# Performance work log

Measured on AMD Instinct MI355X. Metric: run time of the kernel, lower is better.

## Reference

```python
import jax, jax.numpy as jnp
import numpy as np

WH, WW = 8, 8           # window size
NUM_HEADS = 6
DIM = 192
BW = 4096               # num_windows * batch
NW = 64                 # windows per image (mask leading dim)
N = WH * WW             # tokens per window = 64


def _make_rel_coords_table():
    h = np.arange(-(WH - 1), WH, dtype=np.float32)
    w = np.arange(-(WW - 1), WW, dtype=np.float32)
    gh, gw = np.meshgrid(h, w, indexing='ij')
    tbl = np.stack([gh, gw], axis=-1)[None]            # (1, 2Wh-1, 2Ww-1, 2)
    tbl[..., 0] /= (WH - 1)
    tbl[..., 1] /= (WW - 1)
    tbl *= 8.0
    tbl = np.sign(tbl) * np.log2(np.abs(tbl) + 1.0) / np.log2(8.0)
    return jnp.asarray(tbl, dtype=jnp.float32)


def _make_rel_pos_index():
    ch, cw = np.meshgrid(np.arange(WH), np.arange(WW), indexing='ij')
    coords = np.stack([ch, cw]).reshape(2, -1)          # (2, N)
    rel = coords[:, :, None] - coords[:, None, :]       # (2, N, N)
    rel = rel.transpose(1, 2, 0)
    rel[..., 0] += WH - 1
    rel[..., 1] += WW - 1
    rel[..., 0] *= 2 * WW - 1
    return jnp.asarray(rel.sum(-1), dtype=jnp.int64)    # (N, N)


def setup_inputs() -> dict:
    key = jax.random.key(0)
    ks = jax.random.split(key, 8)
    s = 0.02
    return {
        'x': jax.random.normal(ks[0], (BW, N, DIM), dtype=jnp.float32),
        'mask': jnp.zeros((NW, N, N), dtype=jnp.float32),
        'qkv_w': jax.random.normal(ks[1], (3 * DIM, DIM), dtype=jnp.float32) * s,
        'q_bias': jnp.zeros((DIM,), dtype=jnp.float32),
        'v_bias': jnp.zeros((DIM,), dtype=jnp.float32),
        'logit_scale': jnp.log(10.0 * jnp.ones((NUM_HEADS, 1, 1), dtype=jnp.float32)),
        'cpb_w1': jax.random.normal(ks[2], (512, 2), dtype=jnp.float32) * s,
        'cpb_b1': jnp.zeros((512,), dtype=jnp.float32),
        'cpb_w2': jax.random.normal(ks[3], (NUM_HEADS, 512), dtype=jnp.float32) * s,
        'proj_w': jax.random.normal(ks[4], (DIM, DIM), dtype=jnp.float32) * s,
        'proj_b': jnp.zeros((DIM,), dtype=jnp.float32),
        'rel_coords_table': _make_rel_coords_table(),
        'rel_pos_index': _make_rel_pos_index(),
    }


def reference(x, mask, qkv_w, q_bias, v_bias, logit_scale, cpb_w1, cpb_b1,
              cpb_w2, proj_w, proj_b, rel_coords_table, rel_pos_index):
    B_, n, C = x.shape
    H = logit_scale.shape[0]
    d = C // H
    # qkv projection; k has no bias (zeros), matching the torch concat
    qkv_bias = jnp.concatenate([q_bias, jnp.zeros_like(v_bias), v_bias])
    qkv = x @ qkv_w.T + qkv_bias                              # (B_, n, 3C)
    qkv = qkv.reshape(B_, n, 3, H, d).transpose(2, 0, 3, 1, 4)  # (3, B_, H, n, d)
    q, k, v = qkv[0], qkv[1], qkv[2]
    # cosine attention: L2-normalize q, k (eps like F.normalize)
    qn = q / jnp.clip(jnp.linalg.norm(q, axis=-1, keepdims=True), 1e-12)
    kn = k / jnp.clip(jnp.linalg.norm(k, axis=-1, keepdims=True), 1e-12)
    attn = jnp.einsum('bhnd,bhmd->bhnm', qn, kn)              # (B_, H, n, n)
    max_log = jnp.log(jnp.asarray(100.0, dtype=logit_scale.dtype))
    scale = jnp.exp(jnp.minimum(logit_scale, max_log))        # (H,1,1)
    attn = attn * scale
    # continuous position bias via small MLP, gathered by relative index
    hidden = jax.nn.relu(rel_coords_table @ cpb_w1.T + cpb_b1)
    tbl = (hidden @ cpb_w2.T).reshape(-1, H)                  # ((2Wh-1)(2Ww-1), H)
    rpb = tbl[rel_pos_index.reshape(-1)].reshape(n, n, H).transpose(2, 0, 1)
    rpb = 16.0 * jax.nn.sigmoid(rpb)                          # (H, n, n)
    attn = attn + rpb[None]
    nW = mask.shape[0]
    attn = attn.reshape(B_ // nW, nW, H, n, n) + mask[None, :, None]
    attn = jax.nn.softmax(attn.reshape(B_, H, n, n), axis=-1)
    out = jnp.einsum('bhnm,bhmd->bhnd', attn, v)
    out = out.transpose(0, 2, 1, 3).reshape(B_, n, C)
    return out @ proj_w.T + proj_b
```

## Files before the change

### kernel.cpp

```cpp
#include <hip/hip_runtime.h>


#define LDA 200
#define LDV 72
#define LDP 72

typedef __attribute__((ext_vector_type(4))) float floatx4;
typedef __attribute__((ext_vector_type(8))) short shortx8;
typedef __attribute__((ext_vector_type(4))) unsigned short ushortx4;

__device__ __forceinline__ unsigned short f2bf(float f) {
    union { float f; unsigned u; } v; v.f = f;
    return (unsigned short)((v.u + 0x7fffu + ((v.u >> 16) & 1u)) >> 16);
}
__device__ __forceinline__ float bf2f(unsigned short s) {
    union { unsigned u; float f; } v; v.u = ((unsigned)s) << 16;
    return v.f;
}

__global__ void prep_weights(const float* __restrict__ qkv_w,
                             const float* __restrict__ proj_w,
                             const float* __restrict__ q_bias,
                             const float* __restrict__ v_bias,
                             unsigned short* __restrict__ qkvw_bf,
                             unsigned short* __restrict__ projw_bf,
                             float* __restrict__ qkvb) {
    int stride = gridDim.x * blockDim.x;
    for (int i = blockIdx.x * blockDim.x + threadIdx.x; i < 110592 + 36864 + 576; i += stride) {
        if (i < 110592) {
            qkvw_bf[i] = f2bf(qkv_w[i]);
        } else if (i < 110592 + 36864) {
            projw_bf[i - 110592] = f2bf(proj_w[i - 110592]);
        } else {
            int j = i - 110592 - 36864;
            qkvb[j] = (j < 192) ? q_bias[j] : (j < 384 ? 0.f : v_bias[j - 384]);
        }
    }
}

__global__ void prep_cpb_tbl(const float* __restrict__ w1, const float* __restrict__ b1,
                             const float* __restrict__ w2, const float* __restrict__ rct,
                             float* __restrict__ tbls) {
    int wave = threadIdx.x >> 6, lane = threadIdx.x & 63;
    int pr = blockIdx.x * 4 + wave;
    if (pr >= 1350) return;
    int p = pr / 6, h = pr - p * 6;
    float c0 = rct[p * 2], c1 = rct[p * 2 + 1];
    float s = 0.f;
    #pragma unroll
    for (int it = 0; it < 8; ++it) {
        int j = lane + it * 64;
        float hv = fmaxf(0.f, c0 * w1[j * 2] + c1 * w1[j * 2 + 1] + b1[j]);
        s += hv * w2[h * 512 + j];
    }
    #pragma unroll
    for (int off = 32; off >= 1; off >>= 1) s += __shfl_xor(s, off);
    if (lane == 0) tbls[pr] = s;
}

__global__ void prep_cpb_gather(const float* __restrict__ tbls, const int* __restrict__ rpi,
                                float* __restrict__ rpb) {
    int e = blockIdx.x * 256 + threadIdx.x;
    if (e >= 24576) return;
    int stride64 = (rpi[1] == 0) ? 2 : 1;
    int h = e >> 12, rc = e & 4095;
    int idx = rpi[rc * stride64];
    float t = tbls[idx * 6 + h];
    rpb[e] = 16.f / (1.f + __expf(-t));
}

__global__ __launch_bounds__(768, 3) void win_attn(
    const float* __restrict__ x, const float* __restrict__ mask,
    const float* __restrict__ logit_scale,
    const unsigned short* __restrict__ qkvw, const unsigned short* __restrict__ projw,
    const float* __restrict__ qkvb, const float* __restrict__ projb,
    const float* __restrict__ rpb, float* __restrict__ out)
{
    __shared__ unsigned short Xs[64 * LDA];
    __shared__ unsigned short Qs[64 * LDA];
    __shared__ unsigned short Ks[64 * LDA];
    __shared__ unsigned short Vt[192 * LDV];
    __shared__ unsigned short Ps[12][16 * LDP];

    const int tid  = threadIdx.x;
    const int b    = blockIdx.x;
    const int wave = tid >> 6, lane = tid & 63;
    const int c = lane & 15, qd = lane >> 4;

    {
        const float4* xw = (const float4*)(x + (size_t)b * 12288);
        for (int i = tid; i < 3072; i += 768) {
            float4 v = xw[i];
            int token = i / 48, c4 = (i - token * 48) * 4;
            ushortx4 u = { f2bf(v.x), f2bf(v.y), f2bf(v.z), f2bf(v.w) };
            *(ushortx4*)&Xs[token * LDA + c4] = u;
        }
    }
    __syncthreads();

    {
        for (int nti = 0; nti < 3; ++nti) {
            int nt = wave * 3 + nti;
            const unsigned short* bp = qkvw + (nt * 16 + c) * 192 + qd * 8;
            shortx8 bf[6];
            #pragma unroll
            for (int ks = 0; ks < 6; ++ks) bf[ks] = *(const shortx8*)(bp + ks * 32);
            int gcol = nt * 16 + c;
            int part = nt / 12;
            int inner = gcol - part * 192;
            float bias = qkvb[gcol];
            #pragma unroll
            for (int mh = 0; mh < 2; ++mh) {
                shortx8 af[2][6];
                #pragma unroll
                for (int mi = 0; mi < 2; ++mi)
                    #pragma unroll
                    for (int ks = 0; ks < 6; ++ks)
                        af[mi][ks] = *(const shortx8*)&Xs[((mh * 2 + mi) * 16 + c) * LDA + ks * 32 + qd * 8];
                floatx4 acc[2];
                acc[0] = (floatx4){0.f, 0.f, 0.f, 0.f};
                acc[1] = (floatx4){0.f, 0.f, 0.f, 0.f};
                #pragma unroll
                for (int ks = 0; ks < 6; ++ks)
                    #pragma unroll
                    for (int mi = 0; mi < 2; ++mi)
                        acc[mi] = __builtin_amdgcn_mfma_f32_16x16x32_bf16(af[mi][ks], bf[ks], acc[mi], 0, 0, 0);
                #pragma unroll
                for (int mi = 0; mi < 2; ++mi)
                    #pragma unroll
                    for (int r = 0; r < 4; ++r) {
                        int row = (mh * 2 + mi) * 16 + qd * 4 + r;
                        unsigned short bv = f2bf(acc[mi][r] + bias);
                        if (part == 2) Vt[inner * LDV + row] = bv;
                        else if (part == 1) Ks[row * LDA + inner] = bv;
                        else Qs[row * LDA + inner] = bv;
                    }
            }
        }
    }
    __syncthreads();

    {
        int idx = tid;
        int pqk = idx / 384, rem = idx - pqk * 384;
        int h = rem >> 6, token = rem & 63;
        unsigned short* p = (pqk == 0 ? Qs : Ks) + token * LDA + h * 32;
        shortx8 v0 = *(shortx8*)(p),      v1 = *(shortx8*)(p + 8),
                v2 = *(shortx8*)(p + 16), v3 = *(shortx8*)(p + 24);
        float s = 0.f;
        #pragma unroll
        for (int j = 0; j < 8; ++j) {
            float f0 = bf2f((unsigned short)v0[j]), f1 = bf2f((unsigned short)v1[j]);
            float f2 = bf2f((unsigned short)v2[j]), f3 = bf2f((unsigned short)v3[j]);
            s += f0 * f0 + f1 * f1 + f2 * f2 + f3 * f3;
        }
        float rn = 1.f / fmaxf(sqrtf(s), 1e-12f);
        if (pqk == 0) rn *= __expf(fminf(logit_scale[h], 4.605170185988091f));
        #pragma unroll
        for (int j = 0; j < 8; ++j) {
            v0[j] = (short)f2bf(bf2f((unsigned short)v0[j]) * rn);
            v1[j] = (short)f2bf(bf2f((unsigned short)v1[j]) * rn);
            v2[j] = (short)f2bf(bf2f((unsigned short)v2[j]) * rn);
            v3[j] = (short)f2bf(bf2f((unsigned short)v3[j]) * rn);
        }
        *(shortx8*)(p) = v0; *(shortx8*)(p + 8) = v1;
        *(shortx8*)(p + 16) = v2; *(shortx8*)(p + 24) = v3;
    }
    __syncthreads();

    {
        const float* maskw = mask + (size_t)(b & 63) * 4096;
        const int h = wave >> 1;
        const float* rpbh = rpb + h * 4096;
        shortx8 kf[4];
        #pragma unroll
        for (int nt = 0; nt < 4; ++nt)
            kf[nt] = *(const shortx8*)&Ks[(nt * 16 + c) * LDA + h * 32 + qd * 8];
        shortx8 vf[2][2];
        #pragma unroll
        for (int kn = 0; kn < 2; ++kn)
            #pragma unroll
            for (int nd = 0; nd < 2; ++nd)
                vf[kn][nd] = *(const shortx8*)&Vt[(h * 32 + nd * 16 + c) * LDV + kn * 32 + qd * 8];
        #pragma unroll
        for (int mti = 0; mti < 2; ++mti) {
            int mt = (wave & 1) * 2 + mti;
            float rm[4][4];
            #pragma unroll
            for (int r = 0; r < 4; ++r) {
                int row = mt * 16 + qd * 4 + r;
                #pragma unroll
                for (int nt = 0; nt < 4; ++nt) {
                    int col = nt * 16 + c;
                    rm[r][nt] = rpbh[row * 64 + col] + maskw[row * 64 + col];
                }
            }
            shortx8 qf = *(const shortx8*)&Qs[(mt * 16 + c) * LDA + h * 32 + qd * 8];
            floatx4 a[4];
            #pragma unroll
            for (int nt = 0; nt < 4; ++nt) {
                floatx4 z = (floatx4){0.f, 0.f, 0.f, 0.f};
                a[nt] = __builtin_amdgcn_mfma_f32_16x16x32_bf16(qf, kf[nt], z, 0, 0, 0);
            }
            #pragma unroll
            for (int r = 0; r < 4; ++r) {
                float vals[4], vmax = -1e30f;
                #pragma unroll
                for (int nt = 0; nt < 4; ++nt) {
                    float v = a[nt][r] + rm[r][nt];
                    vals[nt] = v; vmax = fmaxf(vmax, v);
                }
                #pragma unroll
                for (int off = 1; off < 16; off <<= 1)
                    vmax = fmaxf(vmax, __shfl_xor(vmax, off, 16));
                float ssum = 0.f;
                #pragma unroll
                for (int nt = 0; nt < 4; ++nt) {
                    float e = __expf(vals[nt] - vmax);
                    vals[nt] = e; ssum += e;
                }
                #pragma unroll
                for (int off = 1; off < 16; off <<= 1)
                    ssum += __shfl_xor(ssum, off, 16);
                float inv = 1.f / ssum;
                #pragma unroll
                for (int nt = 0; nt < 4; ++nt)
                    Ps[wave][(qd * 4 + r) * LDP + nt * 16 + c] = f2bf(vals[nt] * inv);
            }
            asm volatile("s_waitcnt lgkmcnt(0)" ::: "memory");
            shortx8 pf[2];
            #pragma unroll
            for (int kn = 0; kn < 2; ++kn)
                pf[kn] = *(const shortx8*)&Ps[wave][c * LDP + kn * 32 + qd * 8];
            #pragma unroll
            for (int nd = 0; nd < 2; ++nd) {
                floatx4 o = (floatx4){0.f, 0.f, 0.f, 0.f};
                o = __builtin_amdgcn_mfma_f32_16x16x32_bf16(pf[0], vf[0][nd], o, 0, 0, 0);
                o = __builtin_amdgcn_mfma_f32_16x16x32_bf16(pf[1], vf[1][nd], o, 0, 0, 0);
                #pragma unroll
                for (int r = 0; r < 4; ++r)
                    Xs[(mt * 16 + qd * 4 + r) * LDA + h * 32 + nd * 16 + c] = f2bf(o[r]);
            }
        }
    }
    __syncthreads();

    {
        const int nt = wave;
        const unsigned short* bp = projw + (nt * 16 + c) * 192 + qd * 8;
        shortx8 bf[6];
        #pragma unroll
        for (int ks = 0; ks < 6; ++ks) bf[ks] = *(const shortx8*)(bp + ks * 32);
        int gcol = nt * 16 + c;
        float bias = projb[gcol];
        float* outw = out + (size_t)b * 12288;
        #pragma unroll
        for (int mh = 0; mh < 2; ++mh) {
            shortx8 af[2][6];
            #pragma unroll
            for (int mi = 0; mi < 2; ++mi)
                #pragma unroll
                for (int ks = 0; ks < 6; ++ks)
                    af[mi][ks] = *(const shortx8*)&Xs[((mh * 2 + mi) * 16 + c) * LDA + ks * 32 + qd * 8];
            floatx4 acc[2];
            acc[0] = (floatx4){0.f, 0.f, 0.f, 0.f};
            acc[1] = (floatx4){0.f, 0.f, 0.f, 0.f};
            #pragma unroll
            for (int ks = 0; ks < 6; ++ks)
                #pragma unroll
                for (int mi = 0; mi < 2; ++mi)
                    acc[mi] = __builtin_amdgcn_mfma_f32_16x16x32_bf16(af[mi][ks], bf[ks], acc[mi], 0, 0, 0);
            #pragma unroll
            for (int mi = 0; mi < 2; ++mi)
                #pragma unroll
                for (int r = 0; r < 4; ++r)
                    outw[((mh * 2 + mi) * 16 + qd * 4 + r) * 192 + gcol] = acc[mi][r] + bias;
        }
    }
}

extern "C" void kernel_launch(void* const* d_in, const int* in_sizes, int n_in,
                              void* d_out, int out_size, void* d_ws, size_t ws_size,
                              hipStream_t stream) {
    const float* x           = (const float*)d_in[0];
    const float* mask        = (const float*)d_in[1];
    const float* qkv_w       = (const float*)d_in[2];
    const float* q_bias      = (const float*)d_in[3];
    const float* v_bias      = (const float*)d_in[4];
    const float* logit_scale = (const float*)d_in[5];
    const float* cpb_w1      = (const float*)d_in[6];
    const float* cpb_b1      = (const float*)d_in[7];
    const float* cpb_w2      = (const float*)d_in[8];
    const float* proj_w      = (const float*)d_in[9];
    const float* proj_b      = (const float*)d_in[10];
    const float* rct         = (const float*)d_in[11];
    const int*   rpi         = (const int*)d_in[12];

    char* ws = (char*)d_ws;
    unsigned short* qkvw_bf  = (unsigned short*)ws;
    unsigned short* projw_bf = (unsigned short*)(ws + 221184);
    float* qkvb = (float*)(ws + 294912);
    float* rpb  = (float*)(ws + 297216);
    float* tbls = (float*)(ws + 395520);

    prep_weights<<<64, 256, 0, stream>>>(qkv_w, proj_w, q_bias, v_bias, qkvw_bf, projw_bf, qkvb);
    prep_cpb_tbl<<<338, 256, 0, stream>>>(cpb_w1, cpb_b1, cpb_w2, rct, tbls);
    prep_cpb_gather<<<96, 256, 0, stream>>>(tbls, rpi, rpb);
    win_attn<<<4096, 768, 0, stream>>>(x, mask, logit_scale, qkvw_bf, projw_bf,
                                       qkvb, proj_b, rpb, (float*)d_out);
}
```

Before: 590.1 us.

## Spill K/V to global scratch, defer cosine normalization to scores, shrink LDS

K and V projections are no longer kept in LDS. They go to a per-window scratch area inside the output buffer, in MFMA-friendly layouts, and the Ks/Vt shared arrays are removed. Q/K normalization no longer rewrites the vectors. Per-token inverse norms go to LDS and are applied to the QK^T scores. Projection input now reuses Qs, and the launch-bounds occupancy hint is raised. The goal is to cut LDS per block so more blocks can share a CU, at the cost of an extra global/L2 round trip for K and V and possible register pressure from the tighter bound.

```diff
diff --git a/kernel.cpp b/kernel.cpp
--- a/kernel.cpp
+++ b/kernel.cpp
@@ -2,7 +2,6 @@
 
 
 #define LDA 200
-#define LDV 72
 #define LDP 72
 
 typedef __attribute__((ext_vector_type(4))) float floatx4;
@@ -69,7 +68,7 @@
     rpb[e] = 16.f / (1.f + __expf(-t));
 }
 
-__global__ __launch_bounds__(768, 3) void win_attn(
+__global__ __launch_bounds__(768, 6) void win_attn(
     const float* __restrict__ x, const float* __restrict__ mask,
     const float* __restrict__ logit_scale,
     const unsigned short* __restrict__ qkvw, const unsigned short* __restrict__ projw,
@@ -78,14 +77,15 @@
 {
     __shared__ unsigned short Xs[64 * LDA];
     __shared__ unsigned short Qs[64 * LDA];
-    __shared__ unsigned short Ks[64 * LDA];
-    __shared__ unsigned short Vt[192 * LDV];
     __shared__ unsigned short Ps[12][16 * LDP];
 
     const int tid  = threadIdx.x;
     const int b    = blockIdx.x;
     const int wave = tid >> 6, lane = tid & 63;
     const int c = lane & 15, qd = lane >> 4;
+
+    unsigned short* kv = (unsigned short*)(out + (size_t)b * 12288);
+    float* nrm = (float*)Xs;
 
     {
         const float4* xw = (const float4*)(x + (size_t)b * 12288);
@@ -126,28 +126,42 @@
                     for (int mi = 0; mi < 2; ++mi)
                         acc[mi] = __builtin_amdgcn_mfma_f32_16x16x32_bf16(af[mi][ks], bf[ks], acc[mi], 0, 0, 0);
                 #pragma unroll
-                for (int mi = 0; mi < 2; ++mi)
-                    #pragma unroll
-                    for (int r = 0; r < 4; ++r) {
-                        int row = (mh * 2 + mi) * 16 + qd * 4 + r;
-                        unsigned short bv = f2bf(acc[mi][r] + bias);
-                        if (part == 2) Vt[inner * LDV + row] = bv;
-                        else if (part == 1) Ks[row * LDA + inner] = bv;
-                        else Qs[row * LDA + inner] = bv;
+                for (int mi = 0; mi < 2; ++mi) {
+                    int row0 = (mh * 2 + mi) * 16 + qd * 4;
+                    if (part == 2) {
+                        ushortx4 pk;
+                        #pragma unroll
+                        for (int r = 0; r < 4; ++r) pk[r] = f2bf(acc[mi][r] + bias);
+                        *(ushortx4*)&kv[12288 + inner * 64 + row0] = pk;
+                    } else if (part == 1) {
+                        #pragma unroll
+                        for (int r = 0; r < 4; ++r)
+                            kv[(nt - 12) * 1024 + (row0 + r) * 16 + c] = f2bf(acc[mi][r] + bias);
+                    } else {
+                        #pragma unroll
+                        for (int r = 0; r < 4; ++r)
+                            Qs[(row0 + r) * LDA + inner] = f2bf(acc[mi][r] + bias);
                     }
+                }
             }
         }
     }
     __syncthreads();
 
     {
-        int idx = tid;
-        int pqk = idx / 384, rem = idx - pqk * 384;
-        int h = rem >> 6, token = rem & 63;
-        unsigned short* p = (pqk == 0 ? Qs : Ks) + token * LDA + h * 32;
-        shortx8 v0 = *(shortx8*)(p),      v1 = *(shortx8*)(p + 8),
-                v2 = *(shortx8*)(p + 16), v3 = *(shortx8*)(p + 24);
+        int pqk = tid / 384, rem = tid - pqk * 384;
+        int h = rem >> 6, t = rem & 63;
         float s = 0.f;
+        shortx8 v0, v1, v2, v3;
+        if (pqk == 0) {
+            const unsigned short* p = Qs + t * LDA + h * 32;
+            v0 = *(const shortx8*)(p);      v1 = *(const shortx8*)(p + 8);
+            v2 = *(const shortx8*)(p + 16); v3 = *(const shortx8*)(p + 24);
+        } else {
+            const unsigned short* kp = kv + 2 * h * 1024 + t * 16;
+            v0 = *(const shortx8*)(kp);        v1 = *(const shortx8*)(kp + 8);
+            v2 = *(const shortx8*)(kp + 1024); v3 = *(const shortx8*)(kp + 1032);
+        }
         #pragma unroll
         for (int j = 0; j < 8; ++j) {
             float f0 = bf2f((unsigned short)v0[j]), f1 = bf2f((unsigned short)v1[j]);
@@ -156,15 +170,7 @@
         }
         float rn = 1.f / fmaxf(sqrtf(s), 1e-12f);
         if (pqk == 0) rn *= __expf(fminf(logit_scale[h], 4.605170185988091f));
-        #pragma unroll
-        for (int j = 0; j < 8; ++j) {
-            v0[j] = (short)f2bf(bf2f((unsigned short)v0[j]) * rn);
-            v1[j] = (short)f2bf(bf2f((unsigned short)v1[j]) * rn);
-            v2[j] = (short)f2bf(bf2f((unsigned short)v2[j]) * rn);
-            v3[j] = (short)f2bf(bf2f((unsigned short)v3[j]) * rn);
-        }
-        *(shortx8*)(p) = v0; *(shortx8*)(p + 8) = v1;
-        *(shortx8*)(p + 16) = v2; *(shortx8*)(p + 24) = v3;
+        nrm[pqk * 384 + h * 64 + t] = rn;
     }
     __syncthreads();
 
@@ -175,13 +181,16 @@
         shortx8 kf[4];
         #pragma unroll
         for (int nt = 0; nt < 4; ++nt)
-            kf[nt] = *(const shortx8*)&Ks[(nt * 16 + c) * LDA + h * 32 + qd * 8];
+            kf[nt] = *(const shortx8*)&kv[(2 * h + (qd >> 1)) * 1024 + (nt * 16 + c) * 16 + (qd & 1) * 8];
         shortx8 vf[2][2];
         #pragma unroll
         for (int kn = 0; kn < 2; ++kn)
             #pragma unroll
             for (int nd = 0; nd < 2; ++nd)
-                vf[kn][nd] = *(const shortx8*)&Vt[(h * 32 + nd * 16 + c) * LDV + kn * 32 + qd * 8];
+                vf[kn][nd] = *(const shortx8*)&kv[12288 + (h * 32 + nd * 16 + c) * 64 + kn * 32 + qd * 8];
+        float rkc[4];
+        #pragma unroll
+        for (int nt = 0; nt < 4; ++nt) rkc[nt] = nrm[384 + h * 64 + nt * 16 + c];
         #pragma unroll
         for (int mti = 0; mti < 2; ++mti) {
             int mt = (wave & 1) * 2 + mti;
@@ -195,6 +204,9 @@
                     rm[r][nt] = rpbh[row * 64 + col] + maskw[row * 64 + col];
                 }
             }
+            float rqv[4];
+            #pragma unroll
+            for (int r = 0; r < 4; ++r) rqv[r] = nrm[h * 64 + mt * 16 + qd * 4 + r];
             shortx8 qf = *(const shortx8*)&Qs[(mt * 16 + c) * LDA + h * 32 + qd * 8];
             floatx4 a[4];
             #pragma unroll
@@ -207,7 +219,7 @@
                 float vals[4], vmax = -1e30f;
                 #pragma unroll
                 for (int nt = 0; nt < 4; ++nt) {
-                    float v = a[nt][r] + rm[r][nt];
+                    float v = a[nt][r] * rkc[nt] * rqv[r] + rm[r][nt];
                     vals[nt] = v; vmax = fmaxf(vmax, v);
                 }
                 #pragma unroll
@@ -239,7 +251,7 @@
                 o = __builtin_amdgcn_mfma_f32_16x16x32_bf16(pf[1], vf[1][nd], o, 0, 0, 0);
                 #pragma unroll
                 for (int r = 0; r < 4; ++r)
-                    Xs[(mt * 16 + qd * 4 + r) * LDA + h * 32 + nd * 16 + c] = f2bf(o[r]);
+                    Qs[(mt * 16 + qd * 4 + r) * LDA + h * 32 + nd * 16 + c] = f2bf(o[r]);
             }
         }
     }
@@ -261,7 +273,7 @@
             for (int mi = 0; mi < 2; ++mi)
                 #pragma unroll
                 for (int ks = 0; ks < 6; ++ks)
-                    af[mi][ks] = *(const shortx8*)&Xs[((mh * 2 + mi) * 16 + c) * LDA + ks * 32 + qd * 8];
+                    af[mi][ks] = *(const shortx8*)&Qs[((mh * 2 + mi) * 16 + c) * LDA + ks * 32 + qd * 8];
             floatx4 acc[2];
             acc[0] = (floatx4){0.f, 0.f, 0.f, 0.f};
             acc[1] = (floatx4){0.f, 0.f, 0.f, 0.f};
```

After: 864.6 us. 1.47x slower.
